# Kernel tuning notes

Measured on AMD Instinct MI355X. Metric: run time of the kernel, lower is better.

## Reference

```python
import jax, jax.numpy as jnp
import numpy as np

D, NH, NL, NP, DFF = 256, 8, 4, 4, 1024
HD = D // NH
SHAPES = np.array([[100, 152], [50, 76], [25, 38], [13, 19]], dtype=np.int64)
LV = int((SHAPES[:, 0] * SHAPES[:, 1]).sum())  # 20197


def setup_inputs() -> dict:
    key = jax.random.key(0)
    ks = iter(jax.random.split(key, 48))
    bs, Lq = 8, 300

    def w(shape, s=0.02):
        return jax.random.normal(next(ks), shape, jnp.float32) * s

    lsi = np.concatenate([[0], np.cumsum(SHAPES[:, 0] * SHAPES[:, 1])[:-1]]).astype(np.int64)
    return dict(
        tgt=w((bs, Lq, D), 1.0),
        query_pos=w((bs, Lq, D), 1.0),
        reference_points=jax.random.uniform(next(ks), (bs, Lq, NL, 2), jnp.float32),
        src=w((bs, LV, D), 1.0),
        in_proj_w=w((3 * D, D)), in_proj_b=jnp.zeros((3 * D,), jnp.float32),
        out_proj_w=w((D, D)), out_proj_b=jnp.zeros((D,), jnp.float32),
        samp_off_w=w((NH * NL * NP * 2, D)), samp_off_b=w((NH * NL * NP * 2,), 0.5),
        attn_w_w=w((NH * NL * NP, D)), attn_w_b=jnp.zeros((NH * NL * NP,), jnp.float32),
        value_proj_w=w((D, D)), value_proj_b=jnp.zeros((D,), jnp.float32),
        output_proj_w=w((D, D)), output_proj_b=jnp.zeros((D,), jnp.float32),
        lin1_w=w((DFF, D)), lin1_b=jnp.zeros((DFF,), jnp.float32),
        lin2_w=w((D, DFF)), lin2_b=jnp.zeros((D,), jnp.float32),
        norm1_w=jnp.ones((D,), jnp.float32), norm1_b=jnp.zeros((D,), jnp.float32),
        norm2_w=jnp.ones((D,), jnp.float32), norm2_b=jnp.zeros((D,), jnp.float32),
        norm3_w=jnp.ones((D,), jnp.float32), norm3_b=jnp.zeros((D,), jnp.float32),
        spatial_shapes=SHAPES,            # static numpy (shapes must be static)
        level_start_index=lsi,            # static numpy
        padding_mask=jnp.zeros((bs, LV), bool),
    )


def _ln(x, w, b):
    m = x.mean(-1, keepdims=True)
    v = ((x - m) ** 2).mean(-1, keepdims=True)
    return (x - m) * jax.lax.rsqrt(v + 1e-5) * w + b


def _bilinear(vflat, H_, W_, loc):
    # vflat: (b,h,H*W,d); loc: (b,h,q,p,2) normalized to [0,1]
    # matches F.grid_sample(align_corners=False, padding_mode='zeros')
    x = loc[..., 0] * W_ - 0.5
    y = loc[..., 1] * H_ - 0.5
    x0f, y0f = jnp.floor(x), jnp.floor(y)
    lx, ly = x - x0f, y - y0f
    x0, y0 = x0f.astype(jnp.int32), y0f.astype(jnp.int32)
    b, h, q, p = x0.shape

    def gather(ix, iy, wgt):
        valid = (ix >= 0) & (ix < W_) & (iy >= 0) & (iy < H_)
        idx = (jnp.clip(iy, 0, H_ - 1) * W_ + jnp.clip(ix, 0, W_ - 1)).reshape(b, h, q * p)
        g = jnp.take_along_axis(vflat, idx[..., None], axis=2)  # (b,h,q*p,d)
        return g * (wgt * valid).reshape(b, h, q * p, 1)

    out = (gather(x0, y0, (1 - lx) * (1 - ly)) + gather(x0 + 1, y0, lx * (1 - ly))
           + gather(x0, y0 + 1, (1 - lx) * ly) + gather(x0 + 1, y0 + 1, lx * ly))
    return out.reshape(b, h, q, p, -1)


def reference(tgt, query_pos, reference_points, src, in_proj_w, in_proj_b,
              out_proj_w, out_proj_b, samp_off_w, samp_off_b, attn_w_w, attn_w_b,
              value_proj_w, value_proj_b, output_proj_w, output_proj_b,
              lin1_w, lin1_b, lin2_w, lin2_b, norm1_w, norm1_b, norm2_w, norm2_b,
              norm3_w, norm3_b, spatial_shapes, level_start_index, padding_mask):
    bs, Lq, _ = tgt.shape
    ss = np.asarray(spatial_shapes)
    lsi = np.asarray(level_start_index)

    # ---- self attention (eval mode, dropout off) ----
    qk = tgt + query_pos
    qh = (qk @ in_proj_w[:D].T + in_proj_b[:D]).reshape(bs, Lq, NH, HD)
    kh = (qk @ in_proj_w[D:2 * D].T + in_proj_b[D:2 * D]).reshape(bs, Lq, NH, HD)
    vh = (tgt @ in_proj_w[2 * D:].T + in_proj_b[2 * D:]).reshape(bs, Lq, NH, HD)
    scores = jnp.einsum('bqhd,bkhd->bhqk', qh, kh) / jnp.sqrt(jnp.float32(HD))
    attn = jax.nn.softmax(scores, axis=-1)
    sa = jnp.einsum('bhqk,bkhd->bqhd', attn, vh).reshape(bs, Lq, D)
    sa = sa @ out_proj_w.T + out_proj_b
    x = _ln(tgt + sa, norm2_w, norm2_b)

    # ---- MSDeformAttn cross attention ----
    query = x + query_pos
    value = src @ value_proj_w.T + value_proj_b
    value = jnp.where(padding_mask[..., None], 0.0, value)
    value_t = value.reshape(bs, -1, NH, HD).transpose(0, 2, 1, 3)  # (b,h,Lv,d)

    offsets = (query @ samp_off_w.T + samp_off_b).reshape(bs, Lq, NH, NL, NP, 2)
    aw = jax.nn.softmax((query @ attn_w_w.T + attn_w_b).reshape(bs, Lq, NH, NL * NP), -1)
    aw = aw.reshape(bs, Lq, NH, NL, NP)
    norma = jnp.asarray(np.stack([ss[:, 1], ss[:, 0]], -1), jnp.float32)  # (NL,2)=[W,H]
    loc = reference_points[:, :, None, :, None, :] + offsets / norma[None, None, None, :, None, :]

    out = jnp.zeros((bs, Lq, NH, HD), value.dtype)
    for l in range(NL):
        H_, W_ = int(ss[l, 0]), int(ss[l, 1])
        s0 = int(lsi[l])
        vl = value_t[:, :, s0:s0 + H_ * W_]                    # (b,h,HW,d)
        ll = loc[:, :, :, l].transpose(0, 2, 1, 3, 4)          # (b,h,q,p,2)
        samp = _bilinear(vl, H_, W_, ll)                       # (b,h,q,p,d)
        out = out + jnp.einsum('bhqpd,bqhp->bqhd', samp, aw[:, :, :, l])
    ca = out.reshape(bs, Lq, D) @ output_proj_w.T + output_proj_b
    x = _ln(x + ca, norm1_w, norm1_b)

    # ---- FFN ----
    ffn = jax.nn.relu(x @ lin1_w.T + lin1_b) @ lin2_w.T + lin2_b
    x = _ln(x + ffn, norm3_w, norm3_b)
    return (x, loc, aw)
```

## Files before the change

### kernel.cpp

```cpp
#include <hip/hip_runtime.h>
#include <hip/hip_bf16.h>

#define D_ 256
#define NH_ 8
#define HD_ 32
#define NL_ 4
#define NP_ 4
#define DFF_ 1024
#define BS_ 8
#define LQ_ 300
#define LV_ 20197
#define NQ_ (BS_*LQ_)
#define NSRC_ (BS_*LV_*D_)

__device__ __forceinline__ float u2f(unsigned int u) {
    union { unsigned int i; float f; } v; v.i = u << 16; return v.f;
}
__device__ __forceinline__ float lo2f(unsigned int u) {
    union { unsigned int i; float f; } v; v.i = u << 16; return v.f;
}
__device__ __forceinline__ float hi2f(unsigned int u) {
    union { unsigned int i; float f; } v; v.i = u & 0xffff0000u; return v.f;
}
__device__ __forceinline__ unsigned short f2bf_bits(float f) {
    __hip_bfloat16 b = __float2bfloat16(f);
    union { __hip_bfloat16 b; unsigned short u; } v; v.b = b; return v.u;
}

#define DOT4(accum, wv, ap) do { \
    float4 _a = *(const float4*)(ap); \
    accum += wv.x*_a.x + wv.y*_a.y + wv.z*_a.z + wv.w*_a.w; } while(0)

__global__ __launch_bounds__(256) void cvt_bf16_kernel(
    const float* __restrict__ src, unsigned short* __restrict__ vbf)
{
    const int nsrc4 = NSRC_/4;
    for (int i = blockIdx.x*256 + threadIdx.x; i < nsrc4; i += gridDim.x*256) {
        float4 v = ((const float4*)src)[i];
        ushort4 o;
        o.x = f2bf_bits(v.x); o.y = f2bf_bits(v.y);
        o.z = f2bf_bits(v.z); o.w = f2bf_bits(v.w);
        ((ushort4*)vbf)[i] = o;
    }
}

__global__ __launch_bounds__(256) void add_qk_kernel(
    const float* __restrict__ tgt, const float* __restrict__ qp,
    float* __restrict__ qk)
{
    const int i = blockIdx.x*256 + threadIdx.x;
    float4 a = ((const float4*)tgt)[i], b = ((const float4*)qp)[i];
    ((float4*)qk)[i] = make_float4(a.x+b.x, a.y+b.y, a.z+b.z, a.w+b.w);
}

__global__ __launch_bounds__(256) void pack_weights_kernel(
    const float4* __restrict__ ipw,  const float4* __restrict__ opw,
    const float4* __restrict__ sow,  const float4* __restrict__ aww,
    const float4* __restrict__ outw, const float4* __restrict__ l1w,
    const float4* __restrict__ l2w,  const float4* __restrict__ vpw,
    float4* __restrict__ ipwP,  float4* __restrict__ opwP,
    float4* __restrict__ sowP,  float4* __restrict__ awwP,
    float4* __restrict__ outwP, float4* __restrict__ l1wP,
    float4* __restrict__ l2wP,  float4* __restrict__ vpwP)
{
    __shared__ float4 tile[32][33];
    const int RS[8]  = {768,256,256,128,256,1024,256,256};
    const int C4S[8] = {64, 64, 64, 64, 64, 64, 256, 64};
    const int TCUM[9] = {0,48,64,80,88,104,168,232,248};
    int tb = blockIdx.x, mi = 0;
    while (tb >= TCUM[mi+1]) ++mi;
    const int lt = tb - TCUM[mi];
    const float4* in  = (mi==0)?ipw :(mi==1)?opw :(mi==2)?sow :(mi==3)?aww
                       :(mi==4)?outw:(mi==5)?l1w :(mi==6)?l2w :vpw;
    float4* out       = (mi==0)?ipwP:(mi==1)?opwP:(mi==2)?sowP:(mi==3)?awwP
                       :(mi==4)?outwP:(mi==5)?l1wP:(mi==6)?l2wP:vpwP;
    const int R = RS[mi], C4 = C4S[mi];
    const int tpr = C4 >> 5;
    const int by = lt / tpr, bx = lt % tpr;
    const int tx = threadIdx.x & 31, ty = threadIdx.x >> 5;
#pragma unroll
    for (int i = 0; i < 32; i += 8)
        tile[ty+i][tx] = in[(size_t)(by*32+ty+i)*C4 + bx*32+tx];
    __syncthreads();
#pragma unroll
    for (int i = 0; i < 32; i += 8)
        out[(size_t)(bx*32+ty+i)*R + by*32+tx] = tile[tx][ty+i];
}

__global__ __launch_bounds__(256) void qkv_kernel(
    const float* __restrict__ qk, const float* __restrict__ tgt,
    const float4* __restrict__ ipwP, const float* __restrict__ bias,
    float* __restrict__ qh, float* __restrict__ kh, float* __restrict__ vh)
{
    const int t = threadIdx.x, m0 = blockIdx.x * 8, pass = blockIdx.y;
    const float* a0 = ((pass == 2) ? tgt : qk) + (size_t)m0*D_;
    const float4* w4 = ipwP + pass*256 + t;
    float acc[8] = {0,0,0,0,0,0,0,0};
#pragma unroll 4
    for (int c = 0; c < 64; ++c) {
        float4 wv = w4[c*768];
#pragma unroll
        for (int r = 0; r < 8; ++r) DOT4(acc[r], wv, a0 + r*D_ + c*4);
    }
    float bb = bias[pass*256 + t];
    float* dst = (pass == 0) ? qh : (pass == 1) ? kh : vh;
    for (int r = 0; r < 8; ++r) dst[(m0+r)*D_ + t] = acc[r] + bb;
}

__global__ __launch_bounds__(256) void attn_kernel(
    const float* __restrict__ qh, const float* __restrict__ kh,
    const float* __restrict__ vh, float* __restrict__ sa)
{
    __shared__ unsigned short khl[LQ_][HD_+2];
    __shared__ unsigned short vhl[LQ_][HD_+2];
    __shared__ float sc[4][LQ_];
    __shared__ float qbuf[4][HD_];
    const int b = blockIdx.x >> 3, h = blockIdx.x & 7, chunk = blockIdx.y;
    const int t = threadIdx.x, w = t >> 6, lane = t & 63;
    for (int i = t; i < LQ_*HD_; i += 256) {
        int kq = i >> 5, d = i & 31;
        khl[kq][d] = f2bf_bits(kh[(b*LQ_ + kq)*D_ + h*HD_ + d]);
        vhl[kq][d] = f2bf_bits(vh[(b*LQ_ + kq)*D_ + h*HD_ + d]);
    }
    __syncthreads();
    const float scale = 0.17677669529663687f;
    for (int qi = 0; qi < 15; ++qi) {
        const int q = chunk*60 + w*15 + qi;
        if (lane < HD_) qbuf[w][lane] = qh[(b*LQ_ + q)*D_ + h*HD_ + lane];
        float qv[HD_];
#pragma unroll
        for (int d2 = 0; d2 < HD_; ++d2) qv[d2] = qbuf[w][d2];
        float mx = -1e30f;
        for (int k = lane; k < LQ_; k += 64) {
            float s = 0.f;
#pragma unroll
            for (int d2 = 0; d2 < HD_; ++d2) s += qv[d2]*u2f(khl[k][d2]);
            s *= scale;
            sc[w][k] = s;
            mx = fmaxf(mx, s);
        }
#pragma unroll
        for (int off = 32; off; off >>= 1) mx = fmaxf(mx, __shfl_xor(mx, off));
        float lsum = 0.f;
        for (int k = lane; k < LQ_; k += 64) {
            float e = __expf(sc[w][k] - mx);
            sc[w][k] = e; lsum += e;
        }
#pragma unroll
        for (int off = 32; off; off >>= 1) lsum += __shfl_xor(lsum, off);
        const int d = lane & 31, half = lane >> 5;
        float acc = 0.f;
        for (int k = half*150; k < half*150 + 150; ++k) acc += sc[w][k]*u2f(vhl[k][d]);
        acc += __shfl_down(acc, 32);
        if (lane < 32) sa[(b*LQ_ + q)*D_ + h*HD_ + d] = acc / lsum;
    }
}

__global__ __launch_bounds__(256) void proj_res_ln_kernel(
    const float* __restrict__ A, const float4* __restrict__ WP,
    const float* __restrict__ bias, const float* __restrict__ res,
    const float* __restrict__ gw, const float* __restrict__ gb,
    float* __restrict__ out, const float* __restrict__ qp,
    float* __restrict__ outq)
{
    __shared__ float2 part[4][8];
    const int t = threadIdx.x, m0 = blockIdx.x * 8;
    const int w = t >> 6, lane = t & 63;
    const float* a0 = A + (size_t)m0*D_;
    float acc[8] = {0,0,0,0,0,0,0,0};
    const float4* w4 = WP + t;
#pragma unroll 4
    for (int c = 0; c < 64; ++c) {
        float4 wv = w4[c*256];
#pragma unroll
        for (int r = 0; r < 8; ++r) DOT4(acc[r], wv, a0 + r*D_ + c*4);
    }
    const float bb = bias[t], gwv = gw[t], gbv = gb[t];
    float v[8];
#pragma unroll
    for (int r = 0; r < 8; ++r) {
        v[r] = acc[r] + bb + res[(m0+r)*D_+t];
        float s = v[r], ss = v[r]*v[r];
#pragma unroll
        for (int off = 32; off; off >>= 1) {
            s += __shfl_xor(s, off); ss += __shfl_xor(ss, off);
        }
        if (lane == 0) part[w][r] = make_float2(s, ss);
    }
    __syncthreads();
#pragma unroll
    for (int r = 0; r < 8; ++r) {
        float2 p0 = part[0][r], p1 = part[1][r], p2 = part[2][r], p3 = part[3][r];
        float mean = (p0.x+p1.x+p2.x+p3.x) * (1.0f/256.0f);
        float ex2  = (p0.y+p1.y+p2.y+p3.y) * (1.0f/256.0f);
        float var  = ex2 - mean*mean;
        float o = (v[r]-mean) * rsqrtf(var + 1e-5f) * gwv + gbv;
        out[(m0+r)*D_+t] = o;
        if (outq) outq[(m0+r)*D_+t] = o + qp[(m0+r)*D_+t];
    }
}

__global__ __launch_bounds__(256) void samp_params_kernel(
    const float* __restrict__ x1q,
    const float4* __restrict__ sowP, const float* __restrict__ so_b,
    const float4* __restrict__ awwP, const float* __restrict__ aw_b,
    const float* __restrict__ refp,
    float* __restrict__ loc_out, float* __restrict__ aw_out)
{
    __shared__ float logits[8][128];
    const int t = threadIdx.x, m0 = blockIdx.x * 8;
    const float* a0 = x1q + (size_t)m0*D_;
    {
        float acc[8] = {0,0,0,0,0,0,0,0};
        const float4* w4 = sowP + t;
#pragma unroll 4
        for (int c = 0; c < 64; ++c) {
            float4 wv = w4[c*256];
#pragma unroll
            for (int r = 0; r < 8; ++r) DOT4(acc[r], wv, a0 + r*D_ + c*4);
        }
        const float ob = so_b[t];
        const int c_ = t & 1, l_ = (t >> 3) & 3;
        float nrm;
        if (c_ == 0) nrm = (l_==0)?152.f:(l_==1)?76.f:(l_==2)?38.f:19.f;
        else         nrm = (l_==0)?100.f:(l_==1)?50.f:(l_==2)?25.f:13.f;
        for (int r = 0; r < 8; ++r) {
            int m = m0 + r;
            float off = acc[r] + ob;
            loc_out[m*256 + t] = refp[(m*NL_ + l_)*2 + c_] + off / nrm;
        }
    }
    if (t < 128) {
        float acc[8] = {0,0,0,0,0,0,0,0};
        const float4* w4 = awwP + t;
#pragma unroll 4
        for (int c = 0; c < 64; ++c) {
            float4 wv = w4[c*128];
#pragma unroll
            for (int r = 0; r < 8; ++r) DOT4(acc[r], wv, a0 + r*D_ + c*4);
        }
        const float ab = aw_b[t];
        for (int r = 0; r < 8; ++r) logits[r][t] = acc[r] + ab;
    }
    __syncthreads();
    if (t < 128) {
        const int g0 = (t >> 4) << 4;
        for (int r = 0; r < 8; ++r) {
            float mx = -1e30f;
            for (int j = 0; j < 16; ++j) mx = fmaxf(mx, logits[r][g0+j]);
            float s = 0.f;
            for (int j = 0; j < 16; ++j) s += __expf(logits[r][g0+j] - mx);
            aw_out[(m0+r)*128 + t] = __expf(logits[r][t] - mx) / s;
        }
    }
}

__global__ __launch_bounds__(256) void samp_fuse_bf16_kernel(
    const unsigned short* __restrict__ vbf,
    const float* __restrict__ loc_f, const float* __restrict__ aw_f,
    float* __restrict__ svec_g, float* __restrict__ wsum_g)
{
    __shared__ int   cidx[128][4];
    __shared__ float cwt[128][4];
    const int m = blockIdx.x, t = threadIdx.x;
    const int b = m / LQ_;

    if (t < 128) {
        const int l = (t >> 2) & 3;
        const int HS[4] = {100,50,25,13}, WS[4] = {152,76,38,19}, S0[4] = {0,15200,19000,19950};
        const int Hh = HS[l], Ww = WS[l], s0 = S0[l];
        const float aw = aw_f[m*128 + t];
        const float x = loc_f[m*256 + 2*t]*Ww - 0.5f;
        const float y = loc_f[m*256 + 2*t + 1]*Hh - 0.5f;
        const float x0f = floorf(x), y0f = floorf(y);
        const int x0 = (int)x0f, y0 = (int)y0f;
        const float fx = x - x0f, fy = y - y0f;
        const int   cx[4] = {x0, x0+1, x0,   x0+1};
        const int   cy[4] = {y0, y0,   y0+1, y0+1};
        const float cw[4] = {(1.f-fx)*(1.f-fy), fx*(1.f-fy), (1.f-fx)*fy, fx*fy};
        float sw = 0.f;
#pragma unroll
        for (int j = 0; j < 4; ++j) {
            const bool valid = (cx[j] >= 0) & (cx[j] < Ww) & (cy[j] >= 0) & (cy[j] < Hh);
            cidx[t][j] = valid ? (s0 + cy[j]*Ww + cx[j]) : s0;
            float wv = valid ? aw*cw[j] : 0.f;
            cwt[t][j] = wv;
            sw += wv;
        }
#pragma unroll
        for (int off = 8; off; off >>= 1) sw += __shfl_xor(sw, off);
        if ((t & 15) == 0) wsum_g[m*NH_ + (t >> 4)] = sw;
    }
    __syncthreads();

    const int hh = (t >> 7) * 4;
    const int c  = t & 127;
    const unsigned int* sb = (const unsigned int*)(vbf + (size_t)b*LV_*D_) + c;
#pragma unroll
    for (int h = hh; h < hh + 4; ++h) {
        float e0=0.f, e1=0.f, e2=0.f, e3=0.f;
        float o0=0.f, o1=0.f, o2=0.f, o3=0.f;
#pragma unroll 4
        for (int s = 0; s < 16; ++s) {
            const int base = h*16 + s;
            const int   i0 = cidx[base][0], i1 = cidx[base][1],
                        i2 = cidx[base][2], i3 = cidx[base][3];
            const float w0 = cwt[base][0], w1 = cwt[base][1],
                        w2 = cwt[base][2], w3 = cwt[base][3];
            const unsigned int u0 = sb[(size_t)i0*128];
            const unsigned int u1 = sb[(size_t)i1*128];
            const unsigned int u2 = sb[(size_t)i2*128];
            const unsigned int u3 = sb[(size_t)i3*128];
            e0 += w0*lo2f(u0); o0 += w0*hi2f(u0);
            e1 += w1*lo2f(u1); o1 += w1*hi2f(u1);
            e2 += w2*lo2f(u2); o2 += w2*hi2f(u2);
            e3 += w3*lo2f(u3); o3 += w3*hi2f(u3);
        }
        *(float2*)&svec_g[(size_t)m*(NH_*D_) + h*D_ + 2*c] =
            make_float2((e0+e1)+(e2+e3), (o0+o1)+(o2+o3));
    }
}

__global__ __launch_bounds__(256) void vproj_kernel(
    const float* __restrict__ svec_g, const float* __restrict__ wsum_g,
    const float4* __restrict__ vpwP, const float* __restrict__ vpb,
    float* __restrict__ vo)
{
    __shared__ float sv[4][NH_*D_];
    const int t = threadIdx.x, m0 = blockIdx.x * 4;
    for (int i = t; i < 4*NH_*D_; i += 256)
        sv[i >> 11][i & 2047] = svec_g[(size_t)m0*(NH_*D_) + i];
    __syncthreads();
    const int h = t >> 5;
    const float4* w4 = vpwP + t;
    float a0 = 0.f, a1 = 0.f, a2 = 0.f, a3 = 0.f;
    for (int c = 0; c < 64; ++c) {
        const float4 wq = w4[c*256];
        const float4 s0 = *(const float4*)&sv[0][h*D_ + c*4];
        const float4 s1 = *(const float4*)&sv[1][h*D_ + c*4];
        const float4 s2 = *(const float4*)&sv[2][h*D_ + c*4];
        const float4 s3 = *(const float4*)&sv[3][h*D_ + c*4];
        a0 += wq.x*s0.x + wq.y*s0.y + wq.z*s0.z + wq.w*s0.w;
        a1 += wq.x*s1.x + wq.y*s1.y + wq.z*s1.z + wq.w*s1.w;
        a2 += wq.x*s2.x + wq.y*s2.y + wq.z*s2.z + wq.w*s2.w;
        a3 += wq.x*s3.x + wq.y*s3.y + wq.z*s3.z + wq.w*s3.w;
    }
    const float bb = vpb[t];
    vo[(size_t)(m0+0)*D_ + t] = a0 + bb*wsum_g[(m0+0)*NH_ + h];
    vo[(size_t)(m0+1)*D_ + t] = a1 + bb*wsum_g[(m0+1)*NH_ + h];
    vo[(size_t)(m0+2)*D_ + t] = a2 + bb*wsum_g[(m0+2)*NH_ + h];
    vo[(size_t)(m0+3)*D_ + t] = a3 + bb*wsum_g[(m0+3)*NH_ + h];
}

__global__ __launch_bounds__(256) void samp_fuse_f32_kernel(
    const float* __restrict__ src, const float* __restrict__ Wv,
    const float* __restrict__ vpb,
    const float* __restrict__ loc_f, const float* __restrict__ aw_f,
    float* __restrict__ vo)
{
    __shared__ float svec[NH_][D_];
    __shared__ int   cidx[128][4];
    __shared__ float cwt[128][4];
    __shared__ float wsum[NH_];
    const int m = blockIdx.x, t = threadIdx.x;
    const int b = m / LQ_;

    if (t < 128) {
        const int l = (t >> 2) & 3;
        const int HS[4] = {100,50,25,13}, WS[4] = {152,76,38,19}, S0[4] = {0,15200,19000,19950};
        const int Hh = HS[l], Ww = WS[l], s0 = S0[l];
        const float aw = aw_f[m*128 + t];
        const float x = loc_f[m*256 + 2*t]*Ww - 0.5f;
        const float y = loc_f[m*256 + 2*t + 1]*Hh - 0.5f;
        const float x0f = floorf(x), y0f = floorf(y);
        const int x0 = (int)x0f, y0 = (int)y0f;
        const float fx = x - x0f, fy = y - y0f;
        const int   cx[4] = {x0, x0+1, x0,   x0+1};
        const int   cy[4] = {y0, y0,   y0+1, y0+1};
        const float cw[4] = {(1.f-fx)*(1.f-fy), fx*(1.f-fy), (1.f-fx)*fy, fx*fy};
        float sw = 0.f;
#pragma unroll
        for (int jj = 0; jj < 4; ++jj) {
            const bool valid = (cx[jj] >= 0) & (cx[jj] < Ww) & (cy[jj] >= 0) & (cy[jj] < Hh);
            cidx[t][jj] = valid ? (s0 + cy[jj]*Ww + cx[jj]) : s0;
            float wv = valid ? aw*cw[jj] : 0.f;
            cwt[t][jj] = wv;
            sw += wv;
        }
#pragma unroll
        for (int off = 8; off; off >>= 1) sw += __shfl_xor(sw, off);
        if ((t & 15) == 0) wsum[t >> 4] = sw;
    }
    __syncthreads();

    const float* sb = src + (size_t)b*LV_*D_ + t;
#pragma unroll
    for (int h = 0; h < NH_; ++h) {
        float a0 = 0.f, a1 = 0.f, a2 = 0.f, a3 = 0.f;
#pragma unroll 4
        for (int s = 0; s < 16; ++s) {
            const int base = h*16 + s;
            const int   i0 = cidx[base][0], i1 = cidx[base][1],
                        i2 = cidx[base][2], i3 = cidx[base][3];
            const float w0 = cwt[base][0], w1 = cwt[base][1],
                        w2 = cwt[base][2], w3 = cwt[base][3];
            a0 += w0 * sb[(size_t)i0*D_];
            a1 += w1 * sb[(size_t)i1*D_];
            a2 += w2 * sb[(size_t)i2*D_];
            a3 += w3 * sb[(size_t)i3*D_];
        }
        svec[h][t] = (a0 + a1) + (a2 + a3);
    }
    __syncthreads();

    const int h = t >> 5;
    const float4* w4 = (const float4*)(Wv + t*D_);
    float a = 0.f;
    for (int c = 0; c < 64; ++c) {
        float4 wv = w4[c];
        DOT4(a, wv, &svec[h][c*4]);
    }
    vo[m*D_ + t] = a + vpb[t]*wsum[h];
}

__global__ __launch_bounds__(256) void ffn1_kernel(
    const float* __restrict__ x2, const float4* __restrict__ l1wP,
    const float* __restrict__ b1, float* __restrict__ hid)
{
    const int t = threadIdx.x, m0 = blockIdx.x * 8, cc = blockIdx.y;
    const float* a0 = x2 + (size_t)m0*D_;
    const int j = cc*256 + t;
    float acc[8] = {0,0,0,0,0,0,0,0};
    const float4* w4 = l1wP + j;
#pragma unroll 4
    for (int c = 0; c < 64; ++c) {
        float4 wv = w4[c*1024];
#pragma unroll
        for (int r = 0; r < 8; ++r) DOT4(acc[r], wv, a0 + r*D_ + c*4);
    }
    const float bb = b1[j];
    for (int r = 0; r < 8; ++r) {
        float v = acc[r] + bb;
        hid[(m0+r)*DFF_ + j] = v > 0.f ? v : 0.f;
    }
}

__global__ __launch_bounds__(256) void ffn2_ln_kernel(
    const float* __restrict__ hid, const float4* __restrict__ l2wP,
    const float* __restrict__ b2, const float* __restrict__ res,
    const float* __restrict__ gw, const float* __restrict__ gb,
    float* __restrict__ out)
{
    __shared__ float2 part[4][8];
    const int t = threadIdx.x, m0 = blockIdx.x * 8;
    const int w = t >> 6, lane = t & 63;
    const float* h0 = hid + (size_t)m0*DFF_;
    float acc[8] = {0,0,0,0,0,0,0,0};
    const float4* w4 = l2wP + t;
#pragma unroll 4
    for (int c = 0; c < 256; ++c) {
        float4 wv = w4[c*256];
#pragma unroll
        for (int r = 0; r < 8; ++r) DOT4(acc[r], wv, h0 + r*DFF_ + c*4);
    }
    const float bb = b2[t], gwv = gw[t], gbv = gb[t];
    float v[8];
#pragma unroll
    for (int r = 0; r < 8; ++r) {
        v[r] = acc[r] + bb + res[(m0+r)*D_+t];
        float s = v[r], ss = v[r]*v[r];
#pragma unroll
        for (int off = 32; off; off >>= 1) {
            s += __shfl_xor(s, off); ss += __shfl_xor(ss, off);
        }
        if (lane == 0) part[w][r] = make_float2(s, ss);
    }
    __syncthreads();
#pragma unroll
    for (int r = 0; r < 8; ++r) {
        float2 p0 = part[0][r], p1 = part[1][r], p2 = part[2][r], p3 = part[3][r];
        float mean = (p0.x+p1.x+p2.x+p3.x) * (1.0f/256.0f);
        float ex2  = (p0.y+p1.y+p2.y+p3.y) * (1.0f/256.0f);
        float var  = ex2 - mean*mean;
        out[(m0+r)*D_+t] = (v[r]-mean) * rsqrtf(var + 1e-5f) * gwv + gbv;
    }
}

extern "C" void kernel_launch(void* const* d_in, const int* in_sizes, int n_in,
                              void* d_out, int out_size, void* d_ws, size_t ws_size,
                              hipStream_t stream) {
    (void)in_sizes; (void)n_in; (void)out_size;
    const float* tgt  = (const float*)d_in[0];
    const float* qpos = (const float*)d_in[1];
    const float* refp = (const float*)d_in[2];
    const float* srcp = (const float*)d_in[3];
    const float* ipw  = (const float*)d_in[4];
    const float* ipb  = (const float*)d_in[5];
    const float* opw  = (const float*)d_in[6];
    const float* opb  = (const float*)d_in[7];
    const float* sow  = (const float*)d_in[8];
    const float* sob  = (const float*)d_in[9];
    const float* aww  = (const float*)d_in[10];
    const float* awb  = (const float*)d_in[11];
    const float* vpw  = (const float*)d_in[12];
    const float* vpb  = (const float*)d_in[13];
    const float* outw = (const float*)d_in[14];
    const float* outb = (const float*)d_in[15];
    const float* l1w  = (const float*)d_in[16];
    const float* l1b  = (const float*)d_in[17];
    const float* l2w  = (const float*)d_in[18];
    const float* l2b  = (const float*)d_in[19];
    const float* n1w  = (const float*)d_in[20];
    const float* n1b  = (const float*)d_in[21];
    const float* n2w  = (const float*)d_in[22];
    const float* n2b  = (const float*)d_in[23];
    const float* n3w  = (const float*)d_in[24];
    const float* n3b  = (const float*)d_in[25];

    float* wsf = (float*)d_ws;
    float* qh   = wsf;
    float* kh   = wsf + 614400;
    float* vh   = wsf + 1228800;
    float* sa   = wsf + 1843200;
    float* x1   = wsf + 2457600;
    float* vo   = wsf + 3072000;
    float* x2   = wsf + 3686400;
    float* hid  = wsf + 4300800;
    float* qk   = wsf + 6758400;
    float* x1q  = wsf + 7372800;
    float* P0   = wsf + 7987200;
    float4* ipwP  = (float4*)(P0);
    float4* opwP  = (float4*)(P0 + 196608);
    float4* sowP  = (float4*)(P0 + 262144);
    float4* awwP  = (float4*)(P0 + 327680);
    float4* outwP = (float4*)(P0 + 360448);
    float4* l1wP  = (float4*)(P0 + 425984);
    float4* l2wP  = (float4*)(P0 + 688128);
    float4* vpwP  = (float4*)(P0 + 950272);
    unsigned short* vbf = (unsigned short*)(wsf + 9003008);
    float* svec_g = wsf + 9003008 + 20681728;
    float* wsum_g = svec_g + 4915200;
    const size_t need_bytes = (size_t)(9003008 + 20681728 + 4915200 + 19200) * 4;
    const bool use_bf16 = ws_size >= need_bytes;

    float* xout   = (float*)d_out;
    float* locout = xout + 614400;
    float* awout  = xout + 1228800;

    pack_weights_kernel<<<248, 256, 0, stream>>>(
        (const float4*)ipw, (const float4*)opw, (const float4*)sow,
        (const float4*)aww, (const float4*)outw, (const float4*)l1w,
        (const float4*)l2w, (const float4*)vpw,
        ipwP, opwP, sowP, awwP, outwP, l1wP, l2wP, vpwP);
    add_qk_kernel<<<600, 256, 0, stream>>>(tgt, qpos, qk);
    if (use_bf16)
        cvt_bf16_kernel<<<2048, 256, 0, stream>>>(srcp, vbf);
    qkv_kernel<<<dim3(NQ_/8, 3), 256, 0, stream>>>(qk, tgt, ipwP, ipb, qh, kh, vh);
    attn_kernel<<<dim3(BS_*NH_, 5), 256, 0, stream>>>(qh, kh, vh, sa);
    proj_res_ln_kernel<<<NQ_/8, 256, 0, stream>>>(sa, opwP, opb, tgt, n2w, n2b,
                                                  x1, qpos, x1q);
    samp_params_kernel<<<NQ_/8, 256, 0, stream>>>(x1q, sowP, sob, awwP, awb, refp,
                                                  locout, awout);
    if (use_bf16) {
        samp_fuse_bf16_kernel<<<NQ_, 256, 0, stream>>>(vbf, locout, awout, svec_g, wsum_g);
        vproj_kernel<<<NQ_/4, 256, 0, stream>>>(svec_g, wsum_g, vpwP, vpb, vo);
    } else {
        samp_fuse_f32_kernel<<<NQ_, 256, 0, stream>>>(srcp, vpw, vpb, locout, awout, vo);
    }
    proj_res_ln_kernel<<<NQ_/8, 256, 0, stream>>>(vo, outwP, outb, x1, n1w, n1b,
                                                  x2, nullptr, nullptr);
    ffn1_kernel<<<dim3(NQ_/8, 4), 256, 0, stream>>>(x2, l1wP, l1b, hid);
    ffn2_ln_kernel<<<NQ_/8, 256, 0, stream>>>(hid, l2wP, l2b, x2, n3w, n3b, xout);
}
```

Baseline: 656.4 us.

## Move QKV and FFN GEMMs to bf16 MFMA kernels with bf16 operands

Replaces the scalar fp32 QKV projection and FFN kernels with a generic bf16 MFMA GEMM (16x16x32), fed by a new conversion kernel that casts activations and weights to bf16. The FFN hidden layer is written as bf16, and the final residual plus LayerNorm becomes a separate kernel. The fp32 sampling fallback and the workspace-size check are removed, so the bf16 path always runs. This trades fp32 accuracy for matrix-core throughput and less memory traffic, and adds extra conversion and launch overhead.

```diff
diff --git a/kernel.cpp b/kernel.cpp
--- a/kernel.cpp
+++ b/kernel.cpp
@@ -11,7 +11,11 @@
 #define LQ_ 300
 #define LV_ 20197
 #define NQ_ (BS_*LQ_)
+#define MPAD_ 2432
 #define NSRC_ (BS_*LV_*D_)
+
+typedef short bf16x8 __attribute__((ext_vector_type(8)));
+typedef float f32x4  __attribute__((ext_vector_type(4)));
 
 __device__ __forceinline__ float u2f(unsigned int u) {
     union { unsigned int i; float f; } v; v.i = u << 16; return v.f;
@@ -26,6 +30,10 @@
     __hip_bfloat16 b = __float2bfloat16(f);
     union { __hip_bfloat16 b; unsigned short u; } v; v.b = b; return v.u;
 }
+__device__ __forceinline__ ushort4 cv4(float4 a) {
+    ushort4 o; o.x=f2bf_bits(a.x); o.y=f2bf_bits(a.y); o.z=f2bf_bits(a.z); o.w=f2bf_bits(a.w);
+    return o;
+}
 
 #define DOT4(accum, wv, ap) do { \
     float4 _a = *(const float4*)(ap); \
@@ -36,21 +44,30 @@
 {
     const int nsrc4 = NSRC_/4;
     for (int i = blockIdx.x*256 + threadIdx.x; i < nsrc4; i += gridDim.x*256) {
-        float4 v = ((const float4*)src)[i];
-        ushort4 o;
-        o.x = f2bf_bits(v.x); o.y = f2bf_bits(v.y);
-        o.z = f2bf_bits(v.z); o.w = f2bf_bits(v.w);
-        ((ushort4*)vbf)[i] = o;
-    }
-}
-
-__global__ __launch_bounds__(256) void add_qk_kernel(
-    const float* __restrict__ tgt, const float* __restrict__ qp,
-    float* __restrict__ qk)
+        ((ushort4*)vbf)[i] = cv4(((const float4*)src)[i]);
+    }
+}
+
+__global__ __launch_bounds__(256) void cvt_misc_kernel(
+    const float4* __restrict__ tgt, const float4* __restrict__ qp,
+    const float4* __restrict__ ipw, const float4* __restrict__ l1w,
+    const float4* __restrict__ l2w,
+    ushort4* __restrict__ tgt_bf, ushort4* __restrict__ qk_bf,
+    ushort4* __restrict__ ipw_bf, ushort4* __restrict__ l1w_bf,
+    ushort4* __restrict__ l2w_bf)
 {
     const int i = blockIdx.x*256 + threadIdx.x;
-    float4 a = ((const float4*)tgt)[i], b = ((const float4*)qp)[i];
-    ((float4*)qk)[i] = make_float4(a.x+b.x, a.y+b.y, a.z+b.z, a.w+b.w);
+    if (i < 153600) {
+        float4 a = tgt[i], b = qp[i];
+        tgt_bf[i] = cv4(a);
+        qk_bf[i]  = cv4(make_float4(a.x+b.x, a.y+b.y, a.z+b.z, a.w+b.w));
+    } else if (i < 202752) {
+        int j = i - 153600; ipw_bf[j] = cv4(ipw[j]);
+    } else if (i < 268288) {
+        int j = i - 202752; l1w_bf[j] = cv4(l1w[j]);
+    } else if (i < 333824) {
+        int j = i - 268288; l2w_bf[j] = cv4(l2w[j]);
+    }
 }
 
 __global__ __launch_bounds__(256) void pack_weights_kernel(
@@ -87,24 +104,57 @@
         out[(size_t)(bx*32+ty+i)*R + by*32+tx] = tile[tx][ty+i];
 }
 
-__global__ __launch_bounds__(256) void qkv_kernel(
-    const float* __restrict__ qk, const float* __restrict__ tgt,
-    const float4* __restrict__ ipwP, const float* __restrict__ bias,
-    float* __restrict__ qh, float* __restrict__ kh, float* __restrict__ vh)
-{
-    const int t = threadIdx.x, m0 = blockIdx.x * 8, pass = blockIdx.y;
-    const float* a0 = ((pass == 2) ? tgt : qk) + (size_t)m0*D_;
-    const float4* w4 = ipwP + pass*256 + t;
-    float acc[8] = {0,0,0,0,0,0,0,0};
-#pragma unroll 4
-    for (int c = 0; c < 64; ++c) {
-        float4 wv = w4[c*768];
-#pragma unroll
-        for (int r = 0; r < 8; ++r) DOT4(acc[r], wv, a0 + r*D_ + c*4);
-    }
-    float bb = bias[pass*256 + t];
-    float* dst = (pass == 0) ? qh : (pass == 1) ? kh : vh;
-    for (int r = 0; r < 8; ++r) dst[(m0+r)*D_ + t] = acc[r] + bb;
+__global__ __launch_bounds__(256) void gemm_bf16_kernel(
+    const unsigned short* __restrict__ A,
+    const unsigned short* __restrict__ W,
+    const float* __restrict__ bias,
+    float* __restrict__ out,
+    unsigned short* __restrict__ out_bf,
+    const int K, const int Nld, const int relu)
+{
+    const int t = threadIdx.x, wv = t >> 6, l = t & 63;
+    const int m_base = blockIdx.x*64 + wv*16;
+    const int n_base = blockIdx.y*64;
+    const int lr = l & 15, lg = l >> 4;
+    const unsigned short* ap = A + (size_t)(m_base + lr)*K + lg*8;
+    const unsigned short* wp = W + (size_t)(n_base + lr)*K + lg*8;
+    f32x4 ac0 = {0,0,0,0}, ac1 = {0,0,0,0}, ac2 = {0,0,0,0}, ac3 = {0,0,0,0};
+    for (int k = 0; k < K; k += 32) {
+        bf16x8 a  = *(const bf16x8*)(ap + k);
+        bf16x8 b0 = *(const bf16x8*)(wp + k);
+        bf16x8 b1 = *(const bf16x8*)(wp + (size_t)16*K + k);
+        bf16x8 b2 = *(const bf16x8*)(wp + (size_t)32*K + k);
+        bf16x8 b3 = *(const bf16x8*)(wp + (size_t)48*K + k);
+        ac0 = __builtin_amdgcn_mfma_f32_16x16x32_bf16(a, b0, ac0, 0, 0, 0);
+        ac1 = __builtin_amdgcn_mfma_f32_16x16x32_bf16(a, b1, ac1, 0, 0, 0);
+        ac2 = __builtin_amdgcn_mfma_f32_16x16x32_bf16(a, b2, ac2, 0, 0, 0);
+        ac3 = __builtin_amdgcn_mfma_f32_16x16x32_bf16(a, b3, ac3, 0, 0, 0);
+    }
+    const int orow0 = m_base + lg*4;
+    const int ocol  = n_base + lr;
+    const float b0v = bias[ocol], b1v = bias[ocol+16],
+                b2v = bias[ocol+32], b3v = bias[ocol+48];
+#pragma unroll
+    for (int j = 0; j < 4; ++j) {
+        const int row = orow0 + j;
+        if (row < NQ_) {
+            float v0 = ac0[j] + b0v, v1 = ac1[j] + b1v,
+                  v2 = ac2[j] + b2v, v3 = ac3[j] + b3v;
+            if (relu) {
+                v0 = fmaxf(v0, 0.f); v1 = fmaxf(v1, 0.f);
+                v2 = fmaxf(v2, 0.f); v3 = fmaxf(v3, 0.f);
+            }
+            const size_t base = (size_t)row*Nld + ocol;
+            if (out) {
+                out[base]    = v0; out[base+16] = v1;
+                out[base+32] = v2; out[base+48] = v3;
+            }
+            if (out_bf) {
+                out_bf[base]    = f2bf_bits(v0); out_bf[base+16] = f2bf_bits(v1);
+                out_bf[base+32] = f2bf_bits(v2); out_bf[base+48] = f2bf_bits(v3);
+            }
+        }
+    }
 }
 
 __global__ __launch_bounds__(256) void attn_kernel(
@@ -161,7 +211,7 @@
     const float* __restrict__ bias, const float* __restrict__ res,
     const float* __restrict__ gw, const float* __restrict__ gb,
     float* __restrict__ out, const float* __restrict__ qp,
-    float* __restrict__ outq)
+    float* __restrict__ outq, unsigned short* __restrict__ out_bf)
 {
     __shared__ float2 part[4][8];
     const int t = threadIdx.x, m0 = blockIdx.x * 8;
@@ -196,7 +246,39 @@
         float var  = ex2 - mean*mean;
         float o = (v[r]-mean) * rsqrtf(var + 1e-5f) * gwv + gbv;
         out[(m0+r)*D_+t] = o;
-        if (outq) outq[(m0+r)*D_+t] = o + qp[(m0+r)*D_+t];
+        if (outq)   outq[(m0+r)*D_+t] = o + qp[(m0+r)*D_+t];
+        if (out_bf) out_bf[(m0+r)*D_+t] = f2bf_bits(o);
+    }
+}
+
+__global__ __launch_bounds__(256) void res_ln_kernel(
+    const float* __restrict__ y, const float* __restrict__ res,
+    const float* __restrict__ gw, const float* __restrict__ gb,
+    float* __restrict__ out)
+{
+    __shared__ float2 part[4][8];
+    const int t = threadIdx.x, m0 = blockIdx.x * 8;
+    const int w = t >> 6, lane = t & 63;
+    const float gwv = gw[t], gbv = gb[t];
+    float v[8];
+#pragma unroll
+    for (int r = 0; r < 8; ++r) {
+        v[r] = y[(m0+r)*D_+t] + res[(m0+r)*D_+t];
+        float s = v[r], ss = v[r]*v[r];
+#pragma unroll
+        for (int off = 32; off; off >>= 1) {
+            s += __shfl_xor(s, off); ss += __shfl_xor(ss, off);
+        }
+        if (lane == 0) part[w][r] = make_float2(s, ss);
+    }
+    __syncthreads();
+#pragma unroll
+    for (int r = 0; r < 8; ++r) {
+        float2 p0 = part[0][r], p1 = part[1][r], p2 = part[2][r], p3 = part[3][r];
+        float mean = (p0.x+p1.x+p2.x+p3.x) * (1.0f/256.0f);
+        float ex2  = (p0.y+p1.y+p2.y+p3.y) * (1.0f/256.0f);
+        float var  = ex2 - mean*mean;
+        out[(m0+r)*D_+t] = (v[r]-mean) * rsqrtf(var + 1e-5f) * gwv + gbv;
     }
 }
 
@@ -352,144 +434,10 @@
     vo[(size_t)(m0+3)*D_ + t] = a3 + bb*wsum_g[(m0+3)*NH_ + h];
 }
 
-__global__ __launch_bounds__(256) void samp_fuse_f32_kernel(
-    const float* __restrict__ src, const float* __restrict__ Wv,
-    const float* __restrict__ vpb,
-    const float* __restrict__ loc_f, const float* __restrict__ aw_f,
-    float* __restrict__ vo)
-{
-    __shared__ float svec[NH_][D_];
-    __shared__ int   cidx[128][4];
-    __shared__ float cwt[128][4];
-    __shared__ float wsum[NH_];
-    const int m = blockIdx.x, t = threadIdx.x;
-    const int b = m / LQ_;
-
-    if (t < 128) {
-        const int l = (t >> 2) & 3;
-        const int HS[4] = {100,50,25,13}, WS[4] = {152,76,38,19}, S0[4] = {0,15200,19000,19950};
-        const int Hh = HS[l], Ww = WS[l], s0 = S0[l];
-        const float aw = aw_f[m*128 + t];
-        const float x = loc_f[m*256 + 2*t]*Ww - 0.5f;
-        const float y = loc_f[m*256 + 2*t + 1]*Hh - 0.5f;
-        const float x0f = floorf(x), y0f = floorf(y);
-        const int x0 = (int)x0f, y0 = (int)y0f;
-        const float fx = x - x0f, fy = y - y0f;
-        const int   cx[4] = {x0, x0+1, x0,   x0+1};
-        const int   cy[4] = {y0, y0,   y0+1, y0+1};
-        const float cw[4] = {(1.f-fx)*(1.f-fy), fx*(1.f-fy), (1.f-fx)*fy, fx*fy};
-        float sw = 0.f;
-#pragma unroll
-        for (int jj = 0; jj < 4; ++jj) {
-            const bool valid = (cx[jj] >= 0) & (cx[jj] < Ww) & (cy[jj] >= 0) & (cy[jj] < Hh);
-            cidx[t][jj] = valid ? (s0 + cy[jj]*Ww + cx[jj]) : s0;
-            float wv = valid ? aw*cw[jj] : 0.f;
-            cwt[t][jj] = wv;
-            sw += wv;
-        }
-#pragma unroll
-        for (int off = 8; off; off >>= 1) sw += __shfl_xor(sw, off);
-        if ((t & 15) == 0) wsum[t >> 4] = sw;
-    }
-    __syncthreads();
-
-    const float* sb = src + (size_t)b*LV_*D_ + t;
-#pragma unroll
-    for (int h = 0; h < NH_; ++h) {
-        float a0 = 0.f, a1 = 0.f, a2 = 0.f, a3 = 0.f;
-#pragma unroll 4
-        for (int s = 0; s < 16; ++s) {
-            const int base = h*16 + s;
-            const int   i0 = cidx[base][0], i1 = cidx[base][1],
-                        i2 = cidx[base][2], i3 = cidx[base][3];
-            const float w0 = cwt[base][0], w1 = cwt[base][1],
-                        w2 = cwt[base][2], w3 = cwt[base][3];
-            a0 += w0 * sb[(size_t)i0*D_];
-            a1 += w1 * sb[(size_t)i1*D_];
-            a2 += w2 * sb[(size_t)i2*D_];
-            a3 += w3 * sb[(size_t)i3*D_];
-        }
-        svec[h][t] = (a0 + a1) + (a2 + a3);
-    }
-    __syncthreads();
-
-    const int h = t >> 5;
-    const float4* w4 = (const float4*)(Wv + t*D_);
-    float a = 0.f;
-    for (int c = 0; c < 64; ++c) {
-        float4 wv = w4[c];
-        DOT4(a, wv, &svec[h][c*4]);
-    }
-    vo[m*D_ + t] = a + vpb[t]*wsum[h];
-}
-
-__global__ __launch_bounds__(256) void ffn1_kernel(
-    const float* __restrict__ x2, const float4* __restrict__ l1wP,
-    const float* __restrict__ b1, float* __restrict__ hid)
-{
-    const int t = threadIdx.x, m0 = blockIdx.x * 8, cc = blockIdx.y;
-    const float* a0 = x2 + (size_t)m0*D_;
-    const int j = cc*256 + t;
-    float acc[8] = {0,0,0,0,0,0,0,0};
-    const float4* w4 = l1wP + j;
-#pragma unroll 4
-    for (int c = 0; c < 64; ++c) {
-        float4 wv = w4[c*1024];
-#pragma unroll
-        for (int r = 0; r < 8; ++r) DOT4(acc[r], wv, a0 + r*D_ + c*4);
-    }
-    const float bb = b1[j];
-    for (int r = 0; r < 8; ++r) {
-        float v = acc[r] + bb;
-        hid[(m0+r)*DFF_ + j] = v > 0.f ? v : 0.f;
-    }
-}
-
-__global__ __launch_bounds__(256) void ffn2_ln_kernel(
-    const float* __restrict__ hid, const float4* __restrict__ l2wP,
-    const float* __restrict__ b2, const float* __restrict__ res,
-    const float* __restrict__ gw, const float* __restrict__ gb,
-    float* __restrict__ out)
-{
-    __shared__ float2 part[4][8];
-    const int t = threadIdx.x, m0 = blockIdx.x * 8;
-    const int w = t >> 6, lane = t & 63;
-    const float* h0 = hid + (size_t)m0*DFF_;
-    float acc[8] = {0,0,0,0,0,0,0,0};
-    const float4* w4 = l2wP + t;
-#pragma unroll 4
-    for (int c = 0; c < 256; ++c) {
-        float4 wv = w4[c*256];
-#pragma unroll
-        for (int r = 0; r < 8; ++r) DOT4(acc[r], wv, h0 + r*DFF_ + c*4);
-    }
-    const float bb = b2[t], gwv = gw[t], gbv = gb[t];
-    float v[8];
-#pragma unroll
-    for (int r = 0; r < 8; ++r) {
-        v[r] = acc[r] + bb + res[(m0+r)*D_+t];
-        float s = v[r], ss = v[r]*v[r];
-#pragma unroll
-        for (int off = 32; off; off >>= 1) {
-            s += __shfl_xor(s, off); ss += __shfl_xor(ss, off);
-        }
-        if (lane == 0) part[w][r] = make_float2(s, ss);
-    }
-    __syncthreads();
-#pragma unroll
-    for (int r = 0; r < 8; ++r) {
-        float2 p0 = part[0][r], p1 = part[1][r], p2 = part[2][r], p3 = part[3][r];
-        float mean = (p0.x+p1.x+p2.x+p3.x) * (1.0f/256.0f);
-        float ex2  = (p0.y+p1.y+p2.y+p3.y) * (1.0f/256.0f);
-        float var  = ex2 - mean*mean;
-        out[(m0+r)*D_+t] = (v[r]-mean) * rsqrtf(var + 1e-5f) * gwv + gbv;
-    }
-}
-
 extern "C" void kernel_launch(void* const* d_in, const int* in_sizes, int n_in,
                               void* d_out, int out_size, void* d_ws, size_t ws_size,
                               hipStream_t stream) {
-    (void)in_sizes; (void)n_in; (void)out_size;
+    (void)in_sizes; (void)n_in; (void)out_size; (void)ws_size;
     const float* tgt  = (const float*)d_in[0];
     const float* qpos = (const float*)d_in[1];
     const float* refp = (const float*)d_in[2];
@@ -525,10 +473,9 @@
     float* x1   = wsf + 2457600;
     float* vo   = wsf + 3072000;
     float* x2   = wsf + 3686400;
-    float* hid  = wsf + 4300800;
-    float* qk   = wsf + 6758400;
-    float* x1q  = wsf + 7372800;
-    float* P0   = wsf + 7987200;
+    float* y3   = wsf + 4300800;
+    float* x1q  = wsf + 4915200;
+    float* P0   = wsf + 5529600;
     float4* ipwP  = (float4*)(P0);
     float4* opwP  = (float4*)(P0 + 196608);
     float4* sowP  = (float4*)(P0 + 262144);
@@ -537,11 +484,16 @@
     float4* l1wP  = (float4*)(P0 + 425984);
     float4* l2wP  = (float4*)(P0 + 688128);
     float4* vpwP  = (float4*)(P0 + 950272);
-    unsigned short* vbf = (unsigned short*)(wsf + 9003008);
-    float* svec_g = wsf + 9003008 + 20681728;
+    unsigned short* hid_bf = (unsigned short*)(wsf + 6545408);
+    unsigned short* tgt_bf = (unsigned short*)(wsf + 7790592);
+    unsigned short* qk_bf  = (unsigned short*)(wsf + 8101888);
+    unsigned short* x2_bf  = (unsigned short*)(wsf + 8413184);
+    unsigned short* ipw_bf = (unsigned short*)(wsf + 8724480);
+    unsigned short* l1w_bf = (unsigned short*)(wsf + 8822784);
+    unsigned short* l2w_bf = (unsigned short*)(wsf + 8953856);
+    unsigned short* vbf    = (unsigned short*)(wsf + 9084928);
+    float* svec_g = wsf + 9084928 + 20681728;
     float* wsum_g = svec_g + 4915200;
-    const size_t need_bytes = (size_t)(9003008 + 20681728 + 4915200 + 19200) * 4;
-    const bool use_bf16 = ws_size >= need_bytes;
 
     float* xout   = (float*)d_out;
     float* locout = xout + 614400;
@@ -552,23 +504,27 @@
         (const float4*)aww, (const float4*)outw, (const float4*)l1w,
         (const float4*)l2w, (const float4*)vpw,
         ipwP, opwP, sowP, awwP, outwP, l1wP, l2wP, vpwP);
-    add_qk_kernel<<<600, 256, 0, stream>>>(tgt, qpos, qk);
-    if (use_bf16)
-        cvt_bf16_kernel<<<2048, 256, 0, stream>>>(srcp, vbf);
-    qkv_kernel<<<dim3(NQ_/8, 3), 256, 0, stream>>>(qk, tgt, ipwP, ipb, qh, kh, vh);
+    cvt_misc_kernel<<<1304, 256, 0, stream>>>(
+        (const float4*)tgt, (const float4*)qpos, (const float4*)ipw,
+        (const float4*)l1w, (const float4*)l2w,
+        (ushort4*)tgt_bf, (ushort4*)qk_bf, (ushort4*)ipw_bf,
+        (ushort4*)l1w_bf, (ushort4*)l2w_bf);
+    cvt_bf16_kernel<<<2048, 256, 0, stream>>>(srcp, vbf);
+
+    gemm_bf16_kernel<<<dim3(38, 4), 256, 0, stream>>>(qk_bf,  ipw_bf,          ipb,       qh, nullptr, 256, 256, 0);
+    gemm_bf16_kernel<<<dim3(38, 4), 256, 0, stream>>>(qk_bf,  ipw_bf + 65536,  ipb + 256, kh, nullptr, 256, 256, 0);
+    gemm_bf16_kernel<<<dim3(38, 4), 256, 0, stream>>>(tgt_bf, ipw_bf + 131072, ipb + 512, vh, nullptr, 256, 256, 0);
+
     attn_kernel<<<dim3(BS_*NH_, 5), 256, 0, stream>>>(qh, kh, vh, sa);
     proj_res_ln_kernel<<<NQ_/8, 256, 0, stream>>>(sa, opwP, opb, tgt, n2w, n2b,
-                                                  x1, qpos, x1q);
+                                                  x1, qpos, x1q, nullptr);
     samp_params_kernel<<<NQ_/8, 256, 0, stream>>>(x1q, sowP, sob, awwP, awb, refp,
                                                   locout, awout);
-    if (use_bf16) {
-        samp_fuse_bf16_kernel<<<NQ_, 256, 0, stream>>>(vbf, locout, awout, svec_g, wsum_g);
-        vproj_kernel<<<NQ_/4, 256, 0, stream>>>(svec_g, wsum_g, vpwP, vpb, vo);
-    } else {
-        samp_fuse_f32_kernel<<<NQ_, 256, 0, stream>>>(srcp, vpw, vpb, locout, awout, vo);
-    }
+    samp_fuse_bf16_kernel<<<NQ_, 256, 0, stream>>>(vbf, locout, awout, svec_g, wsum_g);
+    vproj_kernel<<<NQ_/4, 256, 0, stream>>>(svec_g, wsum_g, vpwP, vpb, vo);
     proj_res_ln_kernel<<<NQ_/8, 256, 0, stream>>>(vo, outwP, outb, x1, n1w, n1b,
-                                                  x2, nullptr, nullptr);
-    ffn1_kernel<<<dim3(NQ_/8, 4), 256, 0, stream>>>(x2, l1wP, l1b, hid);
-    ffn2_ln_kernel<<<NQ_/8, 256, 0, stream>>>(hid, l2wP, l2b, x2, n3w, n3b, xout);
-}
+                                                  x2, nullptr, nullptr, x2_bf);
+    gemm_bf16_kernel<<<dim3(38, 16), 256, 0, stream>>>(x2_bf,  l1w_bf, l1b, nullptr, hid_bf, 256, 1024, 1);
+    gemm_bf16_kernel<<<dim3(38, 4),  256, 0, stream>>>(hid_bf, l2w_bf, l2b, y3, nullptr, 1024, 256, 0);
+    res_ln_kernel<<<NQ_/8, 256, 0, stream>>>(y3, x2, n3w, n3b, xout);
+}
```

New measurement: 592.2 us. -9.8%, faster.
